# Kernel optimization log

Measured on AMD Instinct MI355X. Metric: run time of the kernel, lower is better.

Reference implementation:

```python
import jax, jax.numpy as jnp
import numpy as np

# plan steps: (downsample_factor, bins_min, bins_max)
PLAN = [(2, 10, 14), (4, 16, 20)]


def _downsample(x, scale):
    # F.interpolate(mode='linear', align_corners=False, scale_factor=1/scale)
    in_len = x.shape[-1]
    out_len = in_len // scale
    sf = in_len / out_len
    src = jnp.maximum((jnp.arange(out_len, dtype=jnp.float32) + 0.5) * sf - 0.5, 0.0)
    i0 = jnp.floor(src).astype(jnp.int32)
    w = src - i0
    i1 = jnp.minimum(i0 + 1, in_len - 1)
    return x[..., i0] * (1.0 - w) + x[..., i1] * w


def _groupshiftadd(x, g):
    # one FFA butterfly stage with group size g
    B, C, R, nc = x.shape
    xg = x.reshape(B, C, R // g, g, nc)
    i = np.arange(g)
    iA = i // 2
    iB = iA + g // 2
    Bs = (i + 1) // 2
    # roll(v, Bs): y[j] = v[(j - Bs) mod nc]; static gather indices
    col = (np.arange(nc)[None, :] - Bs[:, None]) % nc  # (g, nc)
    a = xg[:, :, :, iA, :]                     # (B,C,G,g,nc)
    b = xg[:, :, :, iB[:, None], col]          # (B,C,G,g,nc) shifted rows
    return (a + b).reshape(B, C, R, nc)


def _forward(x):
    std_dev = jnp.std(x, axis=2, ddof=1)  # torch .std(2) is unbiased
    outs = []
    for ds, bmin, bmax in PLAN:
        down = _downsample(x, ds)
        L = down.shape[-1]
        for bins in range(bmin, bmax):
            trunc = L % bins
            arr = down[:, :, :L - trunc] if trunc else down
            r = arr.reshape(arr.shape[0], arr.shape[1], -1, bins)
            ini_rows = r.shape[2]
            k = int(np.ceil(np.log2(ini_rows)))
            target_rows = 2 ** k
            add = target_rows - ini_rows
            if add:
                pad = jnp.zeros((r.shape[0], r.shape[1], add, bins), r.dtype)
                r = jnp.concatenate([r, pad], axis=2)
            y = r
            for stage in range(1, k + 1):
                y = _groupshiftadd(y, 2 ** stage)
            mx = y.max(axis=3)
            # torch.median returns lower middle element for even sizes
            med = jnp.sort(y, axis=3)[..., (bins - 1) // 2]
            snr = (mx - med) / std_dev[:, :, None] / np.sqrt(float(ini_rows))
            outs.append(snr)  # (B, C, target_rows)
    return jnp.concatenate(outs, axis=2)


def setup_inputs() -> dict:
    key = jax.random.key(0)
    x = jax.random.normal(key, (8, 4, 262144), dtype=jnp.float32)
    return {"x": x}


def reference(x):
    return _forward(x)
```

## Files before the change

### kernel.cpp

```cpp
#include <hip/hip_runtime.h>
#include <cmath>


constexpr int NSEQ    = 32;
constexpr int NLEN    = 262144;
constexpr int OUTROWS = 81920;
constexpr int STDCH   = 32;

constexpr int cilog2(int v) { int r = 0; while (v > 1) { v >>= 1; ++r; } return r; }

constexpr size_t SCROFF[8] = {0, 6291456, 12582912, 18874368,
                              27262976, 29360128, 31981568, 34603008};

__device__ __forceinline__ unsigned bf16rne(float f) {
    unsigned u = __float_as_uint(f);
    return (u + 0x7FFFu + ((u >> 16) & 1u)) >> 16;
}
__device__ __forceinline__ unsigned pk2(float lo, float hi) {
    return bf16rne(lo) | (bf16rne(hi) << 16);
}
__device__ __forceinline__ int swz(int r) { return r ^ (((r >> 4) & 7) << 2); }

__global__ __launch_bounds__(256)
void std_partial(const float* __restrict__ x, float2* __restrict__ part)
{
    const int seq = blockIdx.x, ch = blockIdx.y;
    constexpr int N4 = NLEN / 4 / STDCH;
    const float4* xp = reinterpret_cast<const float4*>(x + (size_t)seq * NLEN) + (size_t)ch * N4;
    float s = 0.f, s2 = 0.f;
    for (int i = threadIdx.x; i < N4; i += 256) {
        float4 v = xp[i];
        s  += (v.x + v.y) + (v.z + v.w);
        s2 += (v.x * v.x + v.y * v.y) + (v.z * v.z + v.w * v.w);
    }
    #pragma unroll
    for (int off = 32; off > 0; off >>= 1) {
        s  += __shfl_down(s, off, 64);
        s2 += __shfl_down(s2, off, 64);
    }
    __shared__ float2 ws[4];
    const int w = threadIdx.x >> 6, l = threadIdx.x & 63;
    if (l == 0) ws[w] = make_float2(s, s2);
    __syncthreads();
    if (threadIdx.x == 0) {
        float a = ws[0].x + ws[1].x + ws[2].x + ws[3].x;
        float b = ws[0].y + ws[1].y + ws[2].y + ws[3].y;
        part[seq * STDCH + ch] = make_float2(a, b);
    }
}

template<int BINS, int G, int HB>
__device__ __forceinline__
void fusedA1ip(float* __restrict__ buf, int Q, int c0)
{
    constexpr int CST = G + 4;
    const int r4 = swz(4 * Q);
    float4 ff[HB + 3];
    #pragma unroll
    for (int j = 0; j < HB + 3; ++j) {
        int cc = c0 - 3 + j;
        if (cc < 0) cc += BINS;
        if (cc >= BINS) cc -= BINS;
        ff[j] = *reinterpret_cast<const float4*>(&buf[cc * CST + r4]);
    }
    __syncthreads();
    #pragma unroll
    for (int i = 0; i < HB; ++i) {
        const int c = c0 + i;
        if (c < BINS) {
            float4 f = ff[i + 3], fm1 = ff[i + 2], fm2 = ff[i + 1], fm3 = ff[i];
            float u0 = f.x + f.y;
            float u1 = f.x + fm1.y;
            float4 o;
            o.x = u0 + (f.z + f.w);
            o.y = u0 + (fm1.z + fm1.w);
            o.z = u1 + (fm1.z + fm2.w);
            o.w = u1 + (fm2.z + fm3.w);
            *reinterpret_cast<float4*>(&buf[c * CST + r4]) = o;
        }
    }
    __syncthreads();
}

template<int BINS, int G, int HB>
__device__ __forceinline__
void fusedAip(float* __restrict__ buf, int s, int Q, int c0)
{
    constexpr int CST = G + 4;
    const int h = 1 << (s - 1), S = 1 << s;
    const int q  = Q & (h - 1);
    const int G2 = (Q >> (s - 1)) << (s + 1);
    const int rA0 = swz(G2 + q),     rA1 = swz(G2 + q + h);
    const int rB0 = swz(G2 + S + q), rB1 = swz(G2 + S + q + h);
    const int vo  = swz(G2 + 4 * q);
    auto mbf = [](int x) { int r = x % BINS; return r < 0 ? r + BINS : r; };
    const int ba1 = mbf(c0 - q - 1);
    const int bb0 = mbf(c0 - 2 * q - 2);
    const int bb1 = mbf(c0 - 3 * q - 3);

    float fa0[HB], fa1[HB + 1], fb0[HB + 2], fb1[HB + 3];
    #pragma unroll
    for (int i = 0; i < HB; ++i) {
        int cc = c0 + i; if (cc >= BINS) cc = BINS - 1;
        fa0[i] = buf[cc * CST + rA0];
    }
    int idx = ba1;
    #pragma unroll
    for (int i = 0; i < HB + 1; ++i) {
        fa1[i] = buf[idx * CST + rA1];
        ++idx; if (idx == BINS) idx = 0;
    }
    idx = bb0;
    #pragma unroll
    for (int i = 0; i < HB + 2; ++i) {
        fb0[i] = buf[idx * CST + rB0];
        ++idx; if (idx == BINS) idx = 0;
    }
    idx = bb1;
    #pragma unroll
    for (int i = 0; i < HB + 3; ++i) {
        fb1[i] = buf[idx * CST + rB1];
        ++idx; if (idx == BINS) idx = 0;
    }
    __syncthreads();
    #pragma unroll
    for (int i = 0; i < HB; ++i) {
        const int c = c0 + i;
        if (c < BINS) {
            float u0 = fa0[i] + fa1[i + 1];
            float u1 = fa0[i] + fa1[i];
            float v0c  = fb0[i + 2] + fb1[i + 3];
            float v0p  = fb0[i + 1] + fb1[i + 2];
            float v1p  = fb0[i + 1] + fb1[i + 1];
            float v1pp = fb0[i]     + fb1[i];
            float4 o; o.x = u0 + v0c; o.y = u0 + v0p; o.z = u1 + v1p; o.w = u1 + v1pp;
            *reinterpret_cast<float4*>(&buf[c * CST + vo]) = o;
        }
    }
    __syncthreads();
}

template<int BINS, int G, int H1>
__device__ __forceinline__
void stage9IP(float* __restrict__ buf, int pr, int c0)
{
    constexpr int CST = G + 4;
    const int sA = swz(pr);
    const int sB = sA + 256;
    const int so = swz(2 * pr);
    const int shift = pr % BINS;

    float ra[H1], rb[H1 + 1];
    #pragma unroll
    for (int i = 0; i < H1; ++i) {
        int cc = c0 + i; if (cc >= BINS) cc = BINS - 1;
        ra[i] = buf[cc * CST + sA];
    }
    int idx = c0 - shift - 1;
    idx %= BINS; if (idx < 0) idx += BINS;
    #pragma unroll
    for (int i = 0; i < H1 + 1; ++i) {
        rb[i] = buf[idx * CST + sB];
        ++idx; if (idx == BINS) idx = 0;
    }
    __syncthreads();
    #pragma unroll
    for (int i = 0; i < H1; ++i) {
        const int c = c0 + i;
        if (c < BINS) {
            float2 o; o.x = ra[i] + rb[i + 1]; o.y = ra[i] + rb[i];
            *reinterpret_cast<float2*>(&buf[c * CST + so]) = o;
        }
    }
    __syncthreads();
}

template<int DS, int BINS, int K, int S0, int CPAD>
__device__ __forceinline__
void passA_body(float* __restrict__ buf, const float* __restrict__ xs,
                unsigned short* __restrict__ scrC, int R, int blk, int sl)
{
    constexpr int G     = 1 << S0;
    constexpr int M     = 1 << (K - S0);
    constexpr int CST   = G + 4;
    constexpr int QUADS = G / 4;
    constexpr int LQ    = cilog2(QUADS);
    constexpr int CHB   = 512 / QUADS;
    constexpr int HB    = (BINS + CHB - 1) / CHB;
    constexpr int CS1   = 512 / (G / 2);
    constexpr int H1    = (BINS + CS1 - 1) / CS1;
    const int t = threadIdx.x;

    const int fmax = max(0, min(G * BINS, R * BINS - blk * G * BINS));
    if (fmax <= 0) return;

    if constexpr (DS == 2) {
        const float4* src4 = reinterpret_cast<const float4*>(xs + 2 * (size_t)blk * G * BINS);
        constexpr int NF4 = G * BINS / 2;
        for (int i = t; i < NF4; i += 512) {
            const int f0 = 2 * i;
            if (f0 < fmax) {
                float4 v = src4[i];
                int lr = f0 / BINS, c = f0 - lr * BINS;
                buf[c * CST + swz(lr)] = 0.5f * (v.x + v.y);
                if (f0 + 1 < fmax) {
                    int c1 = c + 1, lr1 = lr;
                    if (c1 == BINS) { c1 = 0; ++lr1; }
                    buf[c1 * CST + swz(lr1)] = 0.5f * (v.z + v.w);
                }
            }
        }
    } else {
        const float4* src4 = reinterpret_cast<const float4*>(xs + 4 * (size_t)blk * G * BINS);
        constexpr int NF4 = G * BINS;
        for (int i = t; i < NF4; i += 512) {
            if (i < fmax) {
                float4 v = src4[i];
                int lr = i / BINS, c = i - lr * BINS;
                buf[c * CST + swz(lr)] = 0.5f * (v.y + v.z);
            }
        }
    }
    for (int f = fmax + t; f < G * BINS; f += 512) {
        int lr = f / BINS, c = f - lr * BINS;
        buf[c * CST + swz(lr)] = 0.f;
    }
    __syncthreads();

    {
        const int Q  = t & (QUADS - 1);
        const int c0 = (t >> LQ) * HB;
        fusedA1ip<BINS, G, HB>(buf, Q, c0);
        fusedAip<BINS, G, HB>(buf, 3, Q, c0);
        fusedAip<BINS, G, HB>(buf, 5, Q, c0);
        fusedAip<BINS, G, HB>(buf, 7, Q, c0);
    }
    if constexpr (S0 == 9) {
        const int pr  = t & (G / 2 - 1);
        const int c01 = (t >> (S0 - 1)) * H1;
        stage9IP<BINS, G, H1>(buf, pr, c01);
    }

    const float* fin = buf;
    if constexpr (G == 512) {
        const int lr = swz(t);
        unsigned u[CPAD / 2];
        #pragma unroll
        for (int k = 0; k < CPAD / 2; ++k) {
            const int ca = 2 * k, cbn = 2 * k + 1;
            float fa = (ca < BINS)  ? fin[ca * CST + lr]  : 0.f;
            float fb = (cbn < BINS) ? fin[cbn * CST + lr] : 0.f;
            u[k] = pk2(fa, fb);
        }
        unsigned short* dst = scrC + ((size_t)(sl * M + blk) * G + t) * CPAD;
        if constexpr (CPAD == 12) {
            uint2* d2 = reinterpret_cast<uint2*>(dst);
            d2[0] = make_uint2(u[0], u[1]);
            d2[1] = make_uint2(u[2], u[3]);
            d2[2] = make_uint2(u[4], u[5]);
        } else {
            uint4* d4 = reinterpret_cast<uint4*>(dst);
            d4[0] = make_uint4(u[0], u[1], u[2], u[3]);
            d4[1] = make_uint4(u[4], u[5], u[6], u[7]);
        }
    } else {
        const int lrn = t & 255, chh = t >> 8;
        const int lr = swz(lrn);
        constexpr int CH = CPAD / 2;
        unsigned u[CH / 2];
        #pragma unroll
        for (int k = 0; k < CH / 2; ++k) {
            const int ca = chh * CH + 2 * k, cbn = ca + 1;
            float fa = (ca < BINS)  ? fin[ca * CST + lr]  : 0.f;
            float fb = (cbn < BINS) ? fin[cbn * CST + lr] : 0.f;
            u[k] = pk2(fa, fb);
        }
        unsigned short* dst = scrC + ((size_t)(sl * M + blk) * G + lrn) * CPAD + chh * CH;
        if constexpr (CH == 8) {
            *reinterpret_cast<uint4*>(dst) = make_uint4(u[0], u[1], u[2], u[3]);
        } else {
            unsigned* d = reinterpret_cast<unsigned*>(dst);
            #pragma unroll
            for (int k = 0; k < CH / 2; ++k) d[k] = u[k];
        }
    }
}

__global__ __launch_bounds__(512, 6)
void passA_all(const float* __restrict__ x, unsigned short* __restrict__ scr)
{
    __shared__ float buf[13 * 516];
    const int b = blockIdx.x;
    if (b < 4096) {
        const int cfg = b >> 10, r = b & 1023, blk = r & 31, sl = r >> 5;
        const float* xs = x + (size_t)sl * NLEN;
        switch (cfg) {
            case 0: passA_body<2, 10, 14, 9, 12>(buf, xs, scr + SCROFF[0], 13107, blk, sl); break;
            case 1: passA_body<2, 11, 14, 9, 12>(buf, xs, scr + SCROFF[1], 11915, blk, sl); break;
            case 2: passA_body<2, 12, 14, 9, 12>(buf, xs, scr + SCROFF[2], 10922, blk, sl); break;
            default: passA_body<2, 13, 14, 9, 16>(buf, xs, scr + SCROFF[3], 10082, blk, sl); break;
        }
    } else {
        const int b2 = b - 4096;
        const int cfg = b2 >> 9, r = b2 & 511, blk = r & 15, sl = r >> 4;
        const float* xs = x + (size_t)sl * NLEN;
        switch (cfg) {
            case 0: passA_body<4, 16, 12, 8, 16>(buf, xs, scr + SCROFF[4], 4096, blk, sl); break;
            case 1: passA_body<4, 17, 12, 8, 20>(buf, xs, scr + SCROFF[5], 3855, blk, sl); break;
            case 2: passA_body<4, 18, 12, 8, 20>(buf, xs, scr + SCROFF[6], 3640, blk, sl); break;
            default: passA_body<4, 19, 12, 8, 20>(buf, xs, scr + SCROFF[7], 3449, blk, sl); break;
        }
    }
}

template<int BINS, int M, int CST, int HB, int LQ>
__device__ __forceinline__
void fusedB(float* __restrict__ zpg, int s, int p, int sub)
{
    constexpr int QUADS = M / 4;
    const int Q   = sub & (QUADS - 1);
    const int chi = sub >> LQ;
    const int c0  = chi * HB;
    const int h = 1 << (s - 1), S = 1 << s;
    const int q  = Q & (h - 1);
    const int G2 = (Q >> (s - 1)) << (s + 1);
    const int rA0 = G2 + q, rA1 = rA0 + h, rB0 = G2 + S + q, rB1 = rB0 + h;
    const int vo = G2 + 4 * q;
    auto mbf = [](int x, int B) { int r = x % B; return r < 0 ? r + B : r; };
    const int ba1 = mbf(c0 - q - p * h - 1, BINS);
    const int bb0 = mbf(c0 - 2 * q - p * S - 2, BINS);
    const int bb1 = mbf(c0 - 3 * q - p * (S + h) - 3, BINS);

    float fa0[HB], fa1[HB + 1], fb0[HB + 2], fb1[HB + 3];
    #pragma unroll
    for (int i = 0; i < HB; ++i) {
        int cc = c0 + i; if (cc >= BINS) cc = BINS - 1;
        fa0[i] = zpg[cc * CST + rA0];
    }
    int idx = ba1;
    #pragma unroll
    for (int i = 0; i < HB + 1; ++i) {
        fa1[i] = zpg[idx * CST + rA1];
        ++idx; if (idx == BINS) idx = 0;
    }
    idx = bb0;
    #pragma unroll
    for (int i = 0; i < HB + 2; ++i) {
        fb0[i] = zpg[idx * CST + rB0];
        ++idx; if (idx == BINS) idx = 0;
    }
    idx = bb1;
    #pragma unroll
    for (int i = 0; i < HB + 3; ++i) {
        fb1[i] = zpg[idx * CST + rB1];
        ++idx; if (idx == BINS) idx = 0;
    }
    __syncthreads();
    #pragma unroll
    for (int i2 = 0; i2 < HB; ++i2) {
        const int c = c0 + i2;
        if (c < BINS) {
            float u0 = fa0[i2] + fa1[i2 + 1];
            float u1 = fa0[i2] + fa1[i2];
            float v0c  = fb0[i2 + 2] + fb1[i2 + 3];
            float v0p  = fb0[i2 + 1] + fb1[i2 + 2];
            float v1p  = fb0[i2 + 1] + fb1[i2 + 1];
            float v1pp = fb0[i2]     + fb1[i2];
            float4 o; o.x = u0 + v0c; o.y = u0 + v0p; o.z = u1 + v1p; o.w = u1 + v1pp;
            *reinterpret_cast<float4*>(&zpg[c * CST + vo]) = o;
        }
    }
    __syncthreads();
}

template<int BINS, int M, int CST, int HSB, int LP>
__device__ __forceinline__
void singleB(float* __restrict__ zpg, int s, int p, int sub)
{
    constexpr int PAIRSB = M / 2;
    const int pr  = sub & (PAIRSB - 1);
    const int chi = sub >> LP;
    const int c0  = chi * HSB;
    const int half = 1 << (s - 1);
    const int qp = pr & (half - 1);
    const int grpbase = (pr >> (s - 1)) << s;
    const int rA = grpbase + qp, rB = rA + half, ro = grpbase + 2 * qp;
    const int shift = (qp + p * half) % BINS;

    float ra[HSB], rb[HSB + 1];
    #pragma unroll
    for (int i = 0; i < HSB; ++i) {
        int cc = c0 + i; if (cc >= BINS) cc = BINS - 1;
        ra[i] = zpg[cc * CST + rA];
    }
    int idx = c0 - shift - 1;
    idx %= BINS; if (idx < 0) idx += BINS;
    #pragma unroll
    for (int i = 0; i < HSB + 1; ++i) {
        rb[i] = zpg[idx * CST + rB];
        ++idx; if (idx == BINS) idx = 0;
    }
    __syncthreads();
    #pragma unroll
    for (int i2 = 0; i2 < HSB; ++i2) {
        const int c = c0 + i2;
        if (c < BINS) {
            float2 o; o.x = ra[i2] + rb[i2 + 1]; o.y = ra[i2] + rb[i2];
            *reinterpret_cast<float2*>(&zpg[c * CST + ro]) = o;
        }
    }
    __syncthreads();
}

template<int BINS, int K, int S0, int CPAD, int OUTOFF>
__device__ __forceinline__
void passB_body(float* __restrict__ zb, float* __restrict__ s_red,
                const unsigned short* __restrict__ scrC, const float2* __restrict__ part,
                float* __restrict__ out, int R, int p_base, int sl)
{
    constexpr int G    = 1 << S0;
    constexpr int M    = 1 << (K - S0);
    constexpr int TS   = K - S0;
    constexpr int P    = 16;
    constexpr int CST  = M + 4;
    constexpr int BCST = BINS * CST;
    constexpr int LQB  = cilog2(M / 4);
    constexpr int CHB  = 32 / (M / 4);
    constexpr int HB   = (BINS + CHB - 1) / CHB;
    constexpr int LPB  = cilog2(M / 2);
    constexpr int CSB  = 32 / (M / 2);
    constexpr int HSB  = (BINS + CSB - 1) / CSB;

    const int t = threadIdx.x;

    if (t < 64) {
        float s = 0.f, s2 = 0.f;
        if (t < 32) { float2 pp = part[sl * STDCH + t]; s = pp.x; s2 = pp.y; }
        #pragma unroll
        for (int off = 16; off > 0; off >>= 1) {
            s  += __shfl_down(s, off, 64);
            s2 += __shfl_down(s2, off, 64);
        }
        if (t == 0) {
            const float n = (float)NLEN;
            s_red[0] = rsqrtf((s2 - s * s / n) / (n - 1.f)) * rsqrtf((float)R);
        }
    }

    {
        constexpr int RUN = P * CPAD / 4;
        constexpr int TOT = M * RUN;
        const int vmax = (R + G - 1) >> S0;
        const unsigned short* base = scrC + (size_t)sl * M * G * CPAD + (size_t)p_base * CPAD;
        for (int i = t; i < TOT; i += 512) {
            const int v = i / RUN, r = i - v * RUN;
            uint2 d = make_uint2(0u, 0u);
            if (v < vmax)
                d = *reinterpret_cast<const uint2*>(base + (size_t)v * G * CPAD + 4 * r);
            const int e0 = 4 * r;
            const int pl = e0 / CPAD, c = e0 - pl * CPAD;
            float* zp = zb + pl * BCST + v;
            if (c + 0 < BINS) zp[(c + 0) * CST] = __uint_as_float(d.x << 16);
            if (c + 1 < BINS) zp[(c + 1) * CST] = __uint_as_float(d.x & 0xFFFF0000u);
            if (c + 2 < BINS) zp[(c + 2) * CST] = __uint_as_float(d.y << 16);
            if (c + 3 < BINS) zp[(c + 3) * CST] = __uint_as_float(d.y & 0xFFFF0000u);
        }
    }
    __syncthreads();

    const int sub = t & 31, pg = t >> 5;
    const int p = p_base + pg;
    float* zpg = zb + pg * BCST;
    fusedB<BINS, M, CST, HB, LQB>(zpg, 1, p, sub);
    fusedB<BINS, M, CST, HB, LQB>(zpg, 3, p, sub);
    if constexpr (TS == 5) {
        singleB<BINS, M, CST, HSB, LPB>(zpg, 5, p, sub);
    }

    constexpr int ROWS = P * M;
    if (t < ROWS) {
        const int pg2 = t >> TS;
        const int v   = t & (M - 1);
        const float* z = zb + pg2 * BCST;
        float a[BINS];
        #pragma unroll
        for (int c = 0; c < BINS; ++c) a[c] = z[c * CST + v];
        float mx = a[0];
        #pragma unroll
        for (int c = 1; c < BINS; ++c) mx = fmaxf(mx, a[c]);
        constexpr int MIDX = (BINS - 1) / 2;
        #pragma unroll
        for (int i = 0; i <= MIDX; ++i) {
            #pragma unroll
            for (int j = i + 1; j < BINS; ++j) {
                float lo = fminf(a[i], a[j]);
                float hi = fmaxf(a[i], a[j]);
                a[i] = lo; a[j] = hi;
            }
        }
        out[(size_t)sl * OUTROWS + OUTOFF + (size_t)p_base * M + t] = (mx - a[MIDX]) * s_red[0];
    }
}

__global__ __launch_bounds__(512, 6)
void passB_all(const unsigned short* __restrict__ scr, const float2* __restrict__ part,
               float* __restrict__ out)
{
    __shared__ float zb[16 * 13 * 36];
    __shared__ float s_red[1];
    const int b = blockIdx.x;
    if (b < 4096) {
        const int cfg = b >> 10, r = b & 1023, pb = r & 31, sl = r >> 5;
        const int p_base = pb * 16;
        switch (cfg) {
            case 0: passB_body<10, 14, 9, 12, 0>    (zb, s_red, scr + SCROFF[0], part, out, 13107, p_base, sl); break;
            case 1: passB_body<11, 14, 9, 12, 16384>(zb, s_red, scr + SCROFF[1], part, out, 11915, p_base, sl); break;
            case 2: passB_body<12, 14, 9, 12, 32768>(zb, s_red, scr + SCROFF[2], part, out, 10922, p_base, sl); break;
            default: passB_body<13, 14, 9, 16, 49152>(zb, s_red, scr + SCROFF[3], part, out, 10082, p_base, sl); break;
        }
    } else {
        const int b2 = b - 4096;
        const int cfg = b2 >> 9, r = b2 & 511, pb = r & 15, sl = r >> 4;
        const int p_base = pb * 16;
        switch (cfg) {
            case 0: passB_body<16, 12, 8, 16, 65536>(zb, s_red, scr + SCROFF[4], part, out, 4096, p_base, sl); break;
            case 1: passB_body<17, 12, 8, 20, 69632>(zb, s_red, scr + SCROFF[5], part, out, 3855, p_base, sl); break;
            case 2: passB_body<18, 12, 8, 20, 73728>(zb, s_red, scr + SCROFF[6], part, out, 3640, p_base, sl); break;
            default: passB_body<19, 12, 8, 20, 77824>(zb, s_red, scr + SCROFF[7], part, out, 3449, p_base, sl); break;
        }
    }
}

extern "C" void kernel_launch(void* const* d_in, const int* in_sizes, int n_in,
                              void* d_out, int out_size, void* d_ws, size_t ws_size,
                              hipStream_t stream)
{
    (void)in_sizes; (void)n_in; (void)out_size; (void)ws_size;
    const float* x = (const float*)d_in[0];
    float* out  = (float*)d_out;
    float* wsf  = (float*)d_ws;
    float2* part = reinterpret_cast<float2*>(wsf + 64);
    unsigned short* scr = reinterpret_cast<unsigned short*>(wsf + 2176);

    hipLaunchKernelGGL(std_partial, dim3(NSEQ, STDCH), dim3(256), 0, stream, x, part);
    hipLaunchKernelGGL(passA_all, dim3(6144), dim3(512), 0, stream, x, scr);
    hipLaunchKernelGGL(passB_all, dim3(6144), dim3(512), 0, stream, scr, part, out);
}
```

Before: 146.7 us.

## Remap threads so early butterfly stages stay wave-local and drop block barriers

Changes the thread-to-(quad, column-chunk) mapping so each wavefront owns a contiguous set of row quads across all its bins. The early FFA stages, whose data dependencies stay inside that row range, then sync with an LDS waitcnt plus a wave barrier instead of __syncthreads. Block-wide barriers are kept for the later stages that cross wave boundaries. This removes several block barriers per tile, but correctness depends on the row-dependency analysis being exact, and the new mapping may change LDS bank-conflict patterns.

```diff
diff --git a/kernel.cpp b/kernel.cpp
--- a/kernel.cpp
+++ b/kernel.cpp
@@ -20,6 +20,21 @@
     return bf16rne(lo) | (bf16rne(hi) << 16);
 }
 __device__ __forceinline__ int swz(int r) { return r ^ (((r >> 4) & 7) << 2); }
+
+__device__ __forceinline__ void wfence()
+{
+    __builtin_amdgcn_sched_barrier(0);
+    asm volatile("s_waitcnt lgkmcnt(0)" ::: "memory");
+    __builtin_amdgcn_sched_barrier(0);
+    __builtin_amdgcn_wave_barrier();
+}
+
+template<bool BAR>
+__device__ __forceinline__ void stsync()
+{
+    if constexpr (BAR) __syncthreads();
+    else wfence();
+}
 
 __global__ __launch_bounds__(256)
 void std_partial(const float* __restrict__ x, float2* __restrict__ part)
@@ -49,7 +64,7 @@
     }
 }
 
-template<int BINS, int G, int HB>
+template<int BINS, int G, int HB, bool BAR>
 __device__ __forceinline__
 void fusedA1ip(float* __restrict__ buf, int Q, int c0)
 {
@@ -63,7 +78,7 @@
         if (cc >= BINS) cc -= BINS;
         ff[j] = *reinterpret_cast<const float4*>(&buf[cc * CST + r4]);
     }
-    __syncthreads();
+    stsync<BAR>();
     #pragma unroll
     for (int i = 0; i < HB; ++i) {
         const int c = c0 + i;
@@ -79,10 +94,10 @@
             *reinterpret_cast<float4*>(&buf[c * CST + r4]) = o;
         }
     }
-    __syncthreads();
-}
-
-template<int BINS, int G, int HB>
+    stsync<BAR>();
+}
+
+template<int BINS, int G, int HB, bool BAR>
 __device__ __forceinline__
 void fusedAip(float* __restrict__ buf, int s, int Q, int c0)
 {
@@ -122,7 +137,7 @@
         fb1[i] = buf[idx * CST + rB1];
         ++idx; if (idx == BINS) idx = 0;
     }
-    __syncthreads();
+    stsync<BAR>();
     #pragma unroll
     for (int i = 0; i < HB; ++i) {
         const int c = c0 + i;
@@ -137,7 +152,7 @@
             *reinterpret_cast<float4*>(&buf[c * CST + vo]) = o;
         }
     }
-    __syncthreads();
+    stsync<BAR>();
 }
 
 template<int BINS, int G, int H1>
@@ -184,8 +199,9 @@
     constexpr int M     = 1 << (K - S0);
     constexpr int CST   = G + 4;
     constexpr int QUADS = G / 4;
-    constexpr int LQ    = cilog2(QUADS);
     constexpr int CHB   = 512 / QUADS;
+    constexpr int LCHB  = cilog2(CHB);
+    constexpr int QPW   = QUADS / 8;
     constexpr int HB    = (BINS + CHB - 1) / CHB;
     constexpr int CS1   = 512 / (G / 2);
     constexpr int H1    = (BINS + CS1 - 1) / CS1;
@@ -228,12 +244,22 @@
     __syncthreads();
 
     {
-        const int Q  = t & (QUADS - 1);
-        const int c0 = (t >> LQ) * HB;
-        fusedA1ip<BINS, G, HB>(buf, Q, c0);
-        fusedAip<BINS, G, HB>(buf, 3, Q, c0);
-        fusedAip<BINS, G, HB>(buf, 5, Q, c0);
-        fusedAip<BINS, G, HB>(buf, 7, Q, c0);
+        const int w = t >> 6, l = t & 63;
+        const int Q  = w * QPW + (l >> LCHB);
+        const int c0 = (l & (CHB - 1)) * HB;
+        if constexpr (S0 == 9) {
+            fusedA1ip<BINS, G, HB, false>(buf, Q, c0);
+            fusedAip <BINS, G, HB, false>(buf, 3, Q, c0);
+            fusedAip <BINS, G, HB, false>(buf, 5, Q, c0);
+            __syncthreads();
+            fusedAip <BINS, G, HB, true >(buf, 7, Q, c0);
+        } else {
+            fusedA1ip<BINS, G, HB, false>(buf, Q, c0);
+            fusedAip <BINS, G, HB, false>(buf, 3, Q, c0);
+            __syncthreads();
+            fusedAip <BINS, G, HB, true >(buf, 5, Q, c0);
+            fusedAip <BINS, G, HB, true >(buf, 7, Q, c0);
+        }
     }
     if constexpr (S0 == 9) {
         const int pr  = t & (G / 2 - 1);
```

Measured after the change: 144.7 us. About the same (-1.3%).
